# Kernel optimization log

Measured on AMD Instinct MI355X. Metric: run time of the kernel, lower is better.

The kernel has to match this reference:

```python
import jax, jax.numpy as jnp
import numpy as np

DIM = 768
HEADS = 12
HEAD_DIM = DIM // HEADS
EPS = 1e-5

def setup_inputs() -> dict:
    key = jax.random.key(0)
    ks = jax.random.split(key, 12)
    s = 1.0 / np.sqrt(DIM)
    x = jax.random.normal(ks[0], (4, 2048, DIM), dtype=jnp.float32)
    Wq = jax.random.uniform(ks[1], (DIM, DIM), jnp.float32, -s, s)
    bq = jnp.zeros((DIM,), jnp.float32)
    Wk = jax.random.uniform(ks[2], (DIM, DIM), jnp.float32, -s, s)
    bk = jnp.zeros((DIM,), jnp.float32)
    Wv = jax.random.uniform(ks[3], (DIM, DIM), jnp.float32, -s, s)
    bv = jnp.zeros((DIM,), jnp.float32)
    W1 = jax.random.uniform(ks[4], (DIM, 2 * DIM), jnp.float32, -s, s)
    b1 = jnp.zeros((2 * DIM,), jnp.float32)
    s2 = 1.0 / np.sqrt(2 * DIM)
    W2 = jax.random.uniform(ks[5], (2 * DIM, DIM), jnp.float32, -s2, s2)
    b2 = jnp.zeros((DIM,), jnp.float32)
    gamma = jnp.ones((DIM,), jnp.float32)
    beta = jnp.zeros((DIM,), jnp.float32)
    return {"x": x, "Wq": Wq, "bq": bq, "Wk": Wk, "bk": bk, "Wv": Wv, "bv": bv,
            "W1": W1, "b1": b1, "W2": W2, "b2": b2, "gamma": gamma, "beta": beta}

def reference(x, Wq, bq, Wk, bk, Wv, bv, W1, b1, W2, b2, gamma, beta):
    B, S, _ = x.shape
    # QKV projections -> (B, H, S, Dh)
    q = (x @ Wq + bq).reshape(B, S, HEADS, HEAD_DIM).transpose(0, 2, 1, 3)
    k = (x @ Wk + bk).reshape(B, S, HEADS, HEAD_DIM).transpose(0, 2, 1, 3)
    v = (x @ Wv + bv).reshape(B, S, HEADS, HEAD_DIM).transpose(0, 2, 1, 3)
    scores = jnp.einsum('bhqd,bhkd->bhqk', q, k) / jnp.sqrt(jnp.float32(HEAD_DIM))
    attn = jax.nn.softmax(scores, axis=-1)  # dropout is identity in eval
    ctx = jnp.einsum('bhqk,bhkd->bhqd', attn, v)
    ctx = ctx.transpose(0, 2, 1, 3).reshape(B, S, DIM)
    # MLP
    out = jax.nn.relu(ctx @ W1 + b1) @ W2 + b2
    # residual + LayerNorm
    h = x + out
    mu = jnp.mean(h, axis=-1, keepdims=True)
    var = jnp.mean(jnp.square(h - mu), axis=-1, keepdims=True)
    return (h - mu) * jax.lax.rsqrt(var + EPS) * gamma + beta
```

## Files before the change

kernel.cpp:

```cpp
#include <hip/hip_runtime.h>
#include <stdint.h>

#define DIM 768
#define HDIM 64
#define NHEADS 12
#define SEQ 2048
#define BATCH 4
#define NTOK (BATCH*SEQ)
#define FF 1536
#define QSCALE 0.1803368801111204f

typedef __bf16 bf16x8 __attribute__((ext_vector_type(8)));
typedef float f32x4 __attribute__((ext_vector_type(4)));
typedef unsigned short u16;
typedef unsigned int u32;

static __device__ __forceinline__ u16 f2bf(float f) {
  u32 u = __float_as_uint(f);
  u32 r = (u + 0x7fffu + ((u >> 16) & 1u)) >> 16;
  return (u16)r;
}

static __device__ __forceinline__ void async16(const void* g, void* l) {
  __builtin_amdgcn_global_load_lds(
      (const __attribute__((address_space(1))) u32*)g,
      (__attribute__((address_space(3))) u32*)l, 16, 0, 0);
}


__global__ void conv_bf16(const float* __restrict__ in, u16* __restrict__ out, int n) {
  int i = (blockIdx.x * 256 + threadIdx.x) * 4;
  if (i < n) {
    float4 f = *(const float4*)(in + i);
    uint2 o;
    o.x = (u32)f2bf(f.x) | ((u32)f2bf(f.y) << 16);
    o.y = (u32)f2bf(f.z) | ((u32)f2bf(f.w) << 16);
    *(uint2*)(out + i) = o;
  }
}

__global__ void transp_bf16(const float* __restrict__ W, u16* __restrict__ Wt, int K, int N) {
  __shared__ float tile[32][33];
  const int k0 = blockIdx.x * 32, n0 = blockIdx.y * 32;
  const int tx = threadIdx.x & 31, ty = threadIdx.x >> 5;
#pragma unroll
  for (int i = 0; i < 4; i++)
    tile[ty + 8 * i][tx] = W[(size_t)(k0 + ty + 8 * i) * N + n0 + tx];
  __syncthreads();
#pragma unroll
  for (int i = 0; i < 4; i++)
    Wt[(size_t)(n0 + ty + 8 * i) * K + k0 + tx] = f2bf(tile[tx][ty + 8 * i]);
}

__global__ void transp_qkv(const float* __restrict__ Wq, const float* __restrict__ Wk,
                           const float* __restrict__ Wv, u16* __restrict__ Wt) {
  __shared__ float tile[32][33];
  const float* W = blockIdx.z == 0 ? Wq : (blockIdx.z == 1 ? Wk : Wv);
  u16* dst = Wt + (size_t)blockIdx.z * DIM * DIM;
  const int k0 = blockIdx.x * 32, n0 = blockIdx.y * 32;
  const int tx = threadIdx.x & 31, ty = threadIdx.x >> 5;
#pragma unroll
  for (int i = 0; i < 4; i++)
    tile[ty + 8 * i][tx] = W[(size_t)(k0 + ty + 8 * i) * DIM + n0 + tx];
  __syncthreads();
#pragma unroll
  for (int i = 0; i < 4; i++)
    dst[(size_t)(n0 + ty + 8 * i) * DIM + k0 + tx] = f2bf(tile[tx][ty + 8 * i]);
}

__global__ void concat_bias(const float* __restrict__ a, const float* __restrict__ b,
                            const float* __restrict__ c, float* __restrict__ o) {
  int i = blockIdx.x * 256 + threadIdx.x;
  if (i < DIM) o[i] = a[i];
  else if (i < 2 * DIM) o[i] = b[i - DIM];
  else if (i < 3 * DIM) o[i] = c[i - 2 * DIM];
}


template<int MODE>
__launch_bounds__(256, 3)
__global__ void gemm128(const u16* __restrict__ A, const u16* __restrict__ Bt,
                        const float* __restrict__ bias, void* __restrict__ outp,
                        int K) {
  __shared__ u16 sA[128 * 64];
  __shared__ u16 sB[128 * 64];
  const int t = threadIdx.x;
  const int w = t >> 6;
  const int lane = t & 63;
  const int quad = lane >> 4;
  const int l15 = lane & 15;
  const int m0 = blockIdx.x * 128;
  const int n0 = blockIdx.y * 128;
  const int wr = (w & 1) * 64;
  const int wc = (w >> 1) * 64;

  f32x4 acc[4][4];
#pragma unroll
  for (int i = 0; i < 4; i++)
#pragma unroll
    for (int j = 0; j < 4; j++) acc[i][j] = (f32x4){0.f, 0.f, 0.f, 0.f};

  const int rowA = lane >> 3;
  const int colSw = ((lane & 7) ^ rowA) * 8;

  for (int k0 = 0; k0 < K; k0 += 64) {
    __syncthreads();
#pragma unroll
    for (int j = 0; j < 4; j++) {
      int r0 = (j * 4 + w) * 8;
      async16(A + (size_t)(m0 + r0 + rowA) * K + k0 + colSw, sA + r0 * 64);
      async16(Bt + (size_t)(n0 + r0 + rowA) * K + k0 + colSw, sB + r0 * 64);
    }
    __builtin_amdgcn_s_waitcnt(0);
    __syncthreads();
#pragma unroll
    for (int ks = 0; ks < 64; ks += 32) {
      bf16x8 a[4], b[4];
#pragma unroll
      for (int i = 0; i < 4; i++)
        a[i] = *(const bf16x8*)(sA + (wr + i * 16 + l15) * 64 +
                                ((((ks >> 3) + quad) ^ (l15 & 7)) * 8));
#pragma unroll
      for (int j = 0; j < 4; j++)
        b[j] = *(const bf16x8*)(sB + (wc + j * 16 + l15) * 64 +
                                ((((ks >> 3) + quad) ^ (l15 & 7)) * 8));
#pragma unroll
      for (int i = 0; i < 4; i++)
#pragma unroll
        for (int j = 0; j < 4; j++)
          acc[i][j] = __builtin_amdgcn_mfma_f32_16x16x32_bf16(a[i], b[j], acc[i][j], 0, 0, 0);
    }
  }

#pragma unroll
  for (int i = 0; i < 4; i++) {
#pragma unroll
    for (int j = 0; j < 4; j++) {
#pragma unroll
      for (int r = 0; r < 4; r++) {
        int m = m0 + wr + i * 16 + quad * 4 + r;
        int n = n0 + wc + j * 16 + l15;
        float v = acc[i][j][r] + bias[n];
        if (MODE == 5) {
          int b = m >> 11, s = m & 2047;
          u16* o = (u16*)outp;
          if (n < DIM) {
            int h = n >> 6, d = n & 63;
            o[(((size_t)(b * NHEADS + h) * SEQ + s) << 6) + d] = f2bf(v * QSCALE);
          } else if (n < 2 * DIM) {
            int nn = n - DIM, h = nn >> 6, d = nn & 63;
            o[(size_t)NTOK * DIM + (((size_t)(b * NHEADS + h) * SEQ + s) << 6) + d] = f2bf(v);
          } else {
            int nn = n - 2 * DIM, h = nn >> 6, d = nn & 63;
            o[2 * (size_t)NTOK * DIM + ((size_t)(b * NHEADS + h) * HDIM + d) * SEQ + s] = f2bf(v);
          }
        } else if (MODE == 3) {
          ((u16*)outp)[(size_t)m * FF + n] = f2bf(fmaxf(v, 0.f));
        } else {
          ((float*)outp)[(size_t)m * DIM + n] = v;
        }
      }
    }
  }
}


__launch_bounds__(256, 3)
__global__ void attn(const u16* __restrict__ Q, const u16* __restrict__ Kb,
                     const u16* __restrict__ Vt, u16* __restrict__ Ctx) {
  __shared__ u16 sK[128 * 64];
  __shared__ u16 sV[64 * 128];
  __shared__ u16 sP[4][32 * 64];
  const int t = threadIdx.x, w = t >> 6, lane = t & 63;
  const int quad = lane >> 4, l15 = lane & 15;

  const int fid = blockIdx.x;
  const int xcd = fid & 7;
  const int idx = fid >> 3;
  const int bh = xcd + 8 * (idx >> 4);
  const int qb = idx & 15;
  const size_t qkbase = (size_t)bh * SEQ * HDIM;
  const int q0 = qb * 128 + w * 32;

  bf16x8 qf[2][2];
#pragma unroll
  for (int i = 0; i < 2; i++)
#pragma unroll
    for (int ks = 0; ks < 2; ks++)
      qf[i][ks] = *(const bf16x8*)(Q + qkbase + (size_t)(q0 + i * 16 + l15) * HDIM +
                                   ks * 32 + quad * 8);

  f32x4 o[2][4];
#pragma unroll
  for (int i = 0; i < 2; i++)
#pragma unroll
    for (int di = 0; di < 4; di++) o[i][di] = (f32x4){0.f, 0.f, 0.f, 0.f};
  float rs[2] = {0.f, 0.f};

  const int rowK = lane >> 3;
  const int colKsw = ((lane & 7) ^ rowK) * 8;
  const int rowVl = lane >> 4;
  const int chV = lane & 15;
  const int swz = l15 & 7;

  for (int kt = 0; kt < SEQ / 128; kt++) {
    __syncthreads();
#pragma unroll
    for (int j = 0; j < 4; j++) {
      int rk = (j * 4 + w) * 8;
      async16(Kb + qkbase + (size_t)(kt * 128 + rk + rowK) * HDIM + colKsw, sK + rk * 64);
      int rv = (j * 4 + w) * 4;
      int rV = rv + rowVl;
      int cV = (chV ^ (rV & 15)) * 8;
      async16(Vt + qkbase + (size_t)rV * SEQ + kt * 128 + cV, sV + rv * 128);
    }
    __builtin_amdgcn_s_waitcnt(0);
    __syncthreads();

    u16* pw = sP[w];
#pragma unroll
    for (int hh = 0; hh < 2; hh++) {
      f32x4 sc[2][4];
#pragma unroll
      for (int n4 = 0; n4 < 4; n4++) {
        int kr = (hh * 4 + n4) * 16;
        bf16x8 a0 = *(const bf16x8*)(sK + (kr + l15) * 64 + ((quad ^ swz) * 8));
        bf16x8 a1 = *(const bf16x8*)(sK + (kr + l15) * 64 + (((4 + quad) ^ swz) * 8));
#pragma unroll
        for (int i = 0; i < 2; i++) {
          f32x4 c = (f32x4){0.f, 0.f, 0.f, 0.f};
          c = __builtin_amdgcn_mfma_f32_16x16x32_bf16(a0, qf[i][0], c, 0, 0, 0);
          c = __builtin_amdgcn_mfma_f32_16x16x32_bf16(a1, qf[i][1], c, 0, 0, 0);
          sc[i][n4] = c;
        }
      }
#pragma unroll
      for (int i = 0; i < 2; i++) {
        int row = i * 16 + l15;
#pragma unroll
        for (int n4 = 0; n4 < 4; n4++) {
          float p0 = __builtin_amdgcn_exp2f(sc[i][n4][0]);
          float p1 = __builtin_amdgcn_exp2f(sc[i][n4][1]);
          float p2 = __builtin_amdgcn_exp2f(sc[i][n4][2]);
          float p3 = __builtin_amdgcn_exp2f(sc[i][n4][3]);
          rs[i] += (p0 + p1) + (p2 + p3);
          u32 lo = ((__float_as_uint(p0) + 0x8000u) >> 16) |
                   ((__float_as_uint(p1) + 0x8000u) & 0xffff0000u);
          u32 hi = ((__float_as_uint(p2) + 0x8000u) >> 16) |
                   ((__float_as_uint(p3) + 0x8000u) & 0xffff0000u);
          int cp = (n4 * 2 + (quad >> 1)) ^ swz;
          *(uint2*)(pw + row * 64 + cp * 8 + (quad & 1) * 4) = (uint2){lo, hi};
        }
      }
#pragma unroll
      for (int ks = 0; ks < 2; ks++) {
        bf16x8 ap[2];
#pragma unroll
        for (int i = 0; i < 2; i++) {
          int row = i * 16 + l15;
          int cp = (ks * 4 + quad) ^ swz;
          ap[i] = *(const bf16x8*)(pw + row * 64 + cp * 8);
        }
#pragma unroll
        for (int di = 0; di < 4; di++) {
          bf16x8 b = *(const bf16x8*)(sV + (di * 16 + l15) * 128 +
                                      (((hh * 8 + ks * 4 + quad) ^ l15) * 8));
          o[0][di] = __builtin_amdgcn_mfma_f32_16x16x32_bf16(ap[0], b, o[0][di], 0, 0, 0);
          o[1][di] = __builtin_amdgcn_mfma_f32_16x16x32_bf16(ap[1], b, o[1][di], 0, 0, 0);
        }
      }
    }
  }

  float rsum[2];
#pragma unroll
  for (int i = 0; i < 2; i++) {
    float s = rs[i];
    s += __shfl_xor(s, 16);
    s += __shfl_xor(s, 32);
    rsum[i] = s;
  }
  int b = bh / NHEADS, h = bh - b * NHEADS;
#pragma unroll
  for (int i = 0; i < 2; i++) {
#pragma unroll
    for (int r = 0; r < 4; r++) {
      float inv = 1.f / __shfl(rsum[i], quad * 4 + r);
      int q = q0 + i * 16 + quad * 4 + r;
      size_t base = (size_t)(b * SEQ + q) * DIM + h * HDIM;
#pragma unroll
      for (int di = 0; di < 4; di++)
        Ctx[base + di * 16 + l15] = f2bf(o[i][di][r] * inv);
    }
  }
}


__launch_bounds__(64)
__global__ void ln_kernel(const float* __restrict__ x, const float* __restrict__ y,
                          const float* __restrict__ gamma, const float* __restrict__ beta,
                          float* __restrict__ out) {
  const int tok = blockIdx.x;
  const int lane = threadIdx.x;
  const float4* X = (const float4*)(x + (size_t)tok * DIM);
  const float4* Y = (const float4*)(y + (size_t)tok * DIM);
  const float4* G = (const float4*)gamma;
  const float4* Bt = (const float4*)beta;
  float4* O = (float4*)(out + (size_t)tok * DIM);

  float4 h[3];
  float s = 0.f;
#pragma unroll
  for (int i = 0; i < 3; i++) {
    float4 a = X[i * 64 + lane], b = Y[i * 64 + lane];
    h[i].x = a.x + b.x; h[i].y = a.y + b.y; h[i].z = a.z + b.z; h[i].w = a.w + b.w;
    s += h[i].x + h[i].y + h[i].z + h[i].w;
  }
#pragma unroll
  for (int off = 32; off >= 1; off >>= 1) s += __shfl_xor(s, off);
  float mu = s * (1.f / DIM);
  float v = 0.f;
#pragma unroll
  for (int i = 0; i < 3; i++) {
    h[i].x -= mu; h[i].y -= mu; h[i].z -= mu; h[i].w -= mu;
    v += h[i].x * h[i].x + h[i].y * h[i].y + h[i].z * h[i].z + h[i].w * h[i].w;
  }
#pragma unroll
  for (int off = 32; off >= 1; off >>= 1) v += __shfl_xor(v, off);
  float rstd = rsqrtf(v * (1.f / DIM) + 1e-5f);
#pragma unroll
  for (int i = 0; i < 3; i++) {
    float4 g = G[i * 64 + lane], bt = Bt[i * 64 + lane];
    float4 r;
    r.x = h[i].x * rstd * g.x + bt.x;
    r.y = h[i].y * rstd * g.y + bt.y;
    r.z = h[i].z * rstd * g.z + bt.z;
    r.w = h[i].w * rstd * g.w + bt.w;
    O[i * 64 + lane] = r;
  }
}


extern "C" void kernel_launch(void* const* d_in, const int* in_sizes, int n_in,
                              void* d_out, int out_size, void* d_ws, size_t ws_size,
                              hipStream_t stream) {
  const float* x  = (const float*)d_in[0];
  const float* Wq = (const float*)d_in[1];
  const float* bq = (const float*)d_in[2];
  const float* Wk = (const float*)d_in[3];
  const float* bk = (const float*)d_in[4];
  const float* Wv = (const float*)d_in[5];
  const float* bv = (const float*)d_in[6];
  const float* W1 = (const float*)d_in[7];
  const float* b1 = (const float*)d_in[8];
  const float* W2 = (const float*)d_in[9];
  const float* b2 = (const float*)d_in[10];
  const float* gamma = (const float*)d_in[11];
  const float* beta  = (const float*)d_in[12];

  char* ws = (char*)d_ws;
  u16* xb   = (u16*)ws;           ws += (size_t)NTOK * DIM * 2;
  u16* Wqkvt = (u16*)ws;          ws += (size_t)DIM * DIM * 3 * 2;
  u16* W1t  = (u16*)ws;           ws += (size_t)DIM * FF * 2;
  u16* W2t  = (u16*)ws;           ws += (size_t)DIM * FF * 2;
  float* bqkv = (float*)ws;       ws += (size_t)3 * DIM * 4;
  u16* Qb   = (u16*)ws;           ws += (size_t)NTOK * DIM * 2;
  u16* Kbf  = (u16*)ws;           ws += (size_t)NTOK * DIM * 2;
  u16* Vtb  = (u16*)ws;           ws += (size_t)NTOK * DIM * 2;
  u16* Ctx  = (u16*)ws;           ws += (size_t)NTOK * DIM * 2;
  u16* H1   = (u16*)ws;           ws += (size_t)NTOK * FF * 2;
  float* Y2 = (float*)ws;         ws += (size_t)NTOK * DIM * 4;

  conv_bf16<<<(NTOK * DIM) / 1024, 256, 0, stream>>>(x, xb, NTOK * DIM);
  transp_qkv<<<dim3(DIM / 32, DIM / 32, 3), 256, 0, stream>>>(Wq, Wk, Wv, Wqkvt);
  transp_bf16<<<dim3(DIM / 32, FF / 32), 256, 0, stream>>>(W1, W1t, DIM, FF);
  transp_bf16<<<dim3(FF / 32, DIM / 32), 256, 0, stream>>>(W2, W2t, FF, DIM);
  concat_bias<<<9, 256, 0, stream>>>(bq, bk, bv, bqkv);

  gemm128<5><<<dim3(NTOK / 128, 3 * DIM / 128), 256, 0, stream>>>(xb, Wqkvt, bqkv, Qb, DIM);

  attn<<<768, 256, 0, stream>>>(Qb, Kbf, Vtb, Ctx);

  gemm128<3><<<dim3(NTOK / 128, FF / 128), 256, 0, stream>>>(Ctx, W1t, b1, H1, DIM);
  gemm128<4><<<dim3(NTOK / 128, DIM / 128), 256, 0, stream>>>(H1, W2t, b2, Y2, FF);

  ln_kernel<<<NTOK, 64, 0, stream>>>(x, Y2, gamma, beta, (float*)d_out);
}
```

Measured before the change: 311.2 us.

## Register-prefetch GEMM and attention tiles, merge weight prep kernels, use perm packing

Replaces the async global-to-LDS loads in the GEMM and attention kernels with register double-buffering: the next K/V or A/B tile is loaded into registers while the current tile is computed, then stored to LDS at the top of the next iteration. It also fuses the three weight-transpose kernels and the bias-concat kernel into one launch, and packs bf16 pairs with a byte-permute instruction. The intent is to overlap global latency with MFMA work and cut launch overhead, at the cost of more registers, which may reduce occupancy, plus extra LDS store instructions.

```diff
diff --git a/kernel.cpp b/kernel.cpp
--- a/kernel.cpp
+++ b/kernel.cpp
@@ -21,12 +21,6 @@
   return (u16)r;
 }
 
-static __device__ __forceinline__ void async16(const void* g, void* l) {
-  __builtin_amdgcn_global_load_lds(
-      (const __attribute__((address_space(1))) u32*)g,
-      (__attribute__((address_space(3))) u32*)l, 16, 0, 0);
-}
-
 
 __global__ void conv_bf16(const float* __restrict__ in, u16* __restrict__ out, int n) {
   int i = (blockIdx.x * 256 + threadIdx.x) * 4;
@@ -39,41 +33,41 @@
   }
 }
 
-__global__ void transp_bf16(const float* __restrict__ W, u16* __restrict__ Wt, int K, int N) {
-  __shared__ float tile[32][33];
-  const int k0 = blockIdx.x * 32, n0 = blockIdx.y * 32;
+__global__ void prep_weights(const float* __restrict__ Wq, const float* __restrict__ Wk,
+                             const float* __restrict__ Wv, const float* __restrict__ W1,
+                             const float* __restrict__ W2, const float* __restrict__ bq,
+                             const float* __restrict__ bk, const float* __restrict__ bv,
+                             u16* __restrict__ Wqkvt, u16* __restrict__ W1t,
+                             u16* __restrict__ W2t, float* __restrict__ bqkv) {
+  const int bid = blockIdx.x;
+  if (bid >= 4032) {
+    int i = (bid - 4032) * 256 + threadIdx.x;
+    if (i < DIM) bqkv[i] = bq[i];
+    else if (i < 2 * DIM) bqkv[i] = bk[i - DIM];
+    else if (i < 3 * DIM) bqkv[i] = bv[i - 2 * DIM];
+    return;
+  }
+  const float* W; u16* dst; int K, N, tile;
+  if (bid < 1728) {
+    int z = bid / 576, t2 = bid - z * 576;
+    W = z == 0 ? Wq : (z == 1 ? Wk : Wv);
+    dst = Wqkvt + (size_t)z * DIM * DIM; K = DIM; N = DIM; tile = t2;
+  } else if (bid < 2880) {
+    W = W1; dst = W1t; K = DIM; N = FF; tile = bid - 1728;
+  } else {
+    W = W2; dst = W2t; K = FF; N = DIM; tile = bid - 2880;
+  }
+  const int ntx = N / 32;
+  const int k0 = (tile / ntx) * 32, n0 = (tile - (tile / ntx) * ntx) * 32;
+  __shared__ float t32[32][33];
   const int tx = threadIdx.x & 31, ty = threadIdx.x >> 5;
 #pragma unroll
   for (int i = 0; i < 4; i++)
-    tile[ty + 8 * i][tx] = W[(size_t)(k0 + ty + 8 * i) * N + n0 + tx];
+    t32[ty + 8 * i][tx] = W[(size_t)(k0 + ty + 8 * i) * N + n0 + tx];
   __syncthreads();
 #pragma unroll
   for (int i = 0; i < 4; i++)
-    Wt[(size_t)(n0 + ty + 8 * i) * K + k0 + tx] = f2bf(tile[tx][ty + 8 * i]);
-}
-
-__global__ void transp_qkv(const float* __restrict__ Wq, const float* __restrict__ Wk,
-                           const float* __restrict__ Wv, u16* __restrict__ Wt) {
-  __shared__ float tile[32][33];
-  const float* W = blockIdx.z == 0 ? Wq : (blockIdx.z == 1 ? Wk : Wv);
-  u16* dst = Wt + (size_t)blockIdx.z * DIM * DIM;
-  const int k0 = blockIdx.x * 32, n0 = blockIdx.y * 32;
-  const int tx = threadIdx.x & 31, ty = threadIdx.x >> 5;
-#pragma unroll
-  for (int i = 0; i < 4; i++)
-    tile[ty + 8 * i][tx] = W[(size_t)(k0 + ty + 8 * i) * DIM + n0 + tx];
-  __syncthreads();
-#pragma unroll
-  for (int i = 0; i < 4; i++)
-    dst[(size_t)(n0 + ty + 8 * i) * DIM + k0 + tx] = f2bf(tile[tx][ty + 8 * i]);
-}
-
-__global__ void concat_bias(const float* __restrict__ a, const float* __restrict__ b,
-                            const float* __restrict__ c, float* __restrict__ o) {
-  int i = blockIdx.x * 256 + threadIdx.x;
-  if (i < DIM) o[i] = a[i];
-  else if (i < 2 * DIM) o[i] = b[i - DIM];
-  else if (i < 3 * DIM) o[i] = c[i - 2 * DIM];
+    dst[(size_t)(n0 + ty + 8 * i) * K + k0 + tx] = f2bf(t32[tx][ty + 8 * i]);
 }
 
 
@@ -103,16 +97,31 @@
   const int rowA = lane >> 3;
   const int colSw = ((lane & 7) ^ rowA) * 8;
 
+  uint4 areg[4], breg[4];
+#pragma unroll
+  for (int j = 0; j < 4; j++) {
+    int r0 = (j * 4 + w) * 8;
+    areg[j] = *(const uint4*)(A + (size_t)(m0 + r0 + rowA) * K + colSw);
+    breg[j] = *(const uint4*)(Bt + (size_t)(n0 + r0 + rowA) * K + colSw);
+  }
+
   for (int k0 = 0; k0 < K; k0 += 64) {
     __syncthreads();
 #pragma unroll
     for (int j = 0; j < 4; j++) {
       int r0 = (j * 4 + w) * 8;
-      async16(A + (size_t)(m0 + r0 + rowA) * K + k0 + colSw, sA + r0 * 64);
-      async16(Bt + (size_t)(n0 + r0 + rowA) * K + k0 + colSw, sB + r0 * 64);
-    }
-    __builtin_amdgcn_s_waitcnt(0);
+      *(uint4*)(sA + r0 * 64 + lane * 8) = areg[j];
+      *(uint4*)(sB + r0 * 64 + lane * 8) = breg[j];
+    }
     __syncthreads();
+    if (k0 + 64 < K) {
+#pragma unroll
+      for (int j = 0; j < 4; j++) {
+        int r0 = (j * 4 + w) * 8;
+        areg[j] = *(const uint4*)(A + (size_t)(m0 + r0 + rowA) * K + k0 + 64 + colSw);
+        breg[j] = *(const uint4*)(Bt + (size_t)(n0 + r0 + rowA) * K + k0 + 64 + colSw);
+      }
+    }
 #pragma unroll
     for (int ks = 0; ks < 64; ks += 32) {
       bf16x8 a[4], b[4];
@@ -203,19 +212,36 @@
   const int chV = lane & 15;
   const int swz = l15 & 7;
 
+  uint4 kreg[4], vreg[4];
+#pragma unroll
+  for (int j = 0; j < 4; j++) {
+    int rk = (j * 4 + w) * 8;
+    kreg[j] = *(const uint4*)(Kb + qkbase + (size_t)(rk + rowK) * HDIM + colKsw);
+    int rV = (j * 4 + w) * 4 + rowVl;
+    vreg[j] = *(const uint4*)(Vt + qkbase + (size_t)rV * SEQ + ((chV ^ (rV & 15)) * 8));
+  }
+
   for (int kt = 0; kt < SEQ / 128; kt++) {
     __syncthreads();
 #pragma unroll
     for (int j = 0; j < 4; j++) {
       int rk = (j * 4 + w) * 8;
-      async16(Kb + qkbase + (size_t)(kt * 128 + rk + rowK) * HDIM + colKsw, sK + rk * 64);
+      *(uint4*)(sK + rk * 64 + lane * 8) = kreg[j];
       int rv = (j * 4 + w) * 4;
-      int rV = rv + rowVl;
-      int cV = (chV ^ (rV & 15)) * 8;
-      async16(Vt + qkbase + (size_t)rV * SEQ + kt * 128 + cV, sV + rv * 128);
-    }
-    __builtin_amdgcn_s_waitcnt(0);
+      *(uint4*)(sV + rv * 128 + lane * 8) = vreg[j];
+    }
     __syncthreads();
+    if (kt < SEQ / 128 - 1) {
+#pragma unroll
+      for (int j = 0; j < 4; j++) {
+        int rk = (j * 4 + w) * 8;
+        kreg[j] = *(const uint4*)(Kb + qkbase +
+                                  (size_t)((kt + 1) * 128 + rk + rowK) * HDIM + colKsw);
+        int rV = (j * 4 + w) * 4 + rowVl;
+        vreg[j] = *(const uint4*)(Vt + qkbase + (size_t)rV * SEQ + (kt + 1) * 128 +
+                                  ((chV ^ (rV & 15)) * 8));
+      }
+    }
 
     u16* pw = sP[w];
 #pragma unroll
@@ -244,10 +270,10 @@
           float p2 = __builtin_amdgcn_exp2f(sc[i][n4][2]);
           float p3 = __builtin_amdgcn_exp2f(sc[i][n4][3]);
           rs[i] += (p0 + p1) + (p2 + p3);
-          u32 lo = ((__float_as_uint(p0) + 0x8000u) >> 16) |
-                   ((__float_as_uint(p1) + 0x8000u) & 0xffff0000u);
-          u32 hi = ((__float_as_uint(p2) + 0x8000u) >> 16) |
-                   ((__float_as_uint(p3) + 0x8000u) & 0xffff0000u);
+          u32 lo = __builtin_amdgcn_perm(__float_as_uint(p1) + 0x8000u,
+                                         __float_as_uint(p0) + 0x8000u, 0x07060302u);
+          u32 hi = __builtin_amdgcn_perm(__float_as_uint(p3) + 0x8000u,
+                                         __float_as_uint(p2) + 0x8000u, 0x07060302u);
           int cp = (n4 * 2 + (quad >> 1)) ^ swz;
           *(uint2*)(pw + row * 64 + cp * 8 + (quad & 1) * 4) = (uint2){lo, hi};
         }
@@ -372,10 +398,8 @@
   float* Y2 = (float*)ws;         ws += (size_t)NTOK * DIM * 4;
 
   conv_bf16<<<(NTOK * DIM) / 1024, 256, 0, stream>>>(x, xb, NTOK * DIM);
-  transp_qkv<<<dim3(DIM / 32, DIM / 32, 3), 256, 0, stream>>>(Wq, Wk, Wv, Wqkvt);
-  transp_bf16<<<dim3(DIM / 32, FF / 32), 256, 0, stream>>>(W1, W1t, DIM, FF);
-  transp_bf16<<<dim3(FF / 32, DIM / 32), 256, 0, stream>>>(W2, W2t, FF, DIM);
-  concat_bias<<<9, 256, 0, stream>>>(bq, bk, bv, bqkv);
+  prep_weights<<<4041, 256, 0, stream>>>(Wq, Wk, Wv, W1, W2, bq, bk, bv,
+                                         Wqkvt, W1t, W2t, bqkv);
 
   gemm128<5><<<dim3(NTOK / 128, 3 * DIM / 128), 256, 0, stream>>>(xb, Wqkvt, bqkv, Qb, DIM);
 
```

Measured after the change: 636.3 us. +104.5%, slower.
